# Performance work log

Measured on AMD Instinct MI355X. Metric: run time of the kernel, lower is better.

The kernel has to match this reference:

```python
import jax, jax.numpy as jnp
import numpy as np

EPS = 1e-6
NUM_GROUPS = 32


def setup_inputs() -> dict:
    key = jax.random.key(0)
    ks = jax.random.split(key, 10)
    b, c, h, w = 8, 256, 128, 128
    x = jax.random.normal(ks[0], (b, c, h, w), dtype=jnp.float32)
    gamma = jnp.ones((c,), dtype=jnp.float32)
    beta = jnp.zeros((c,), dtype=jnp.float32)
    Wq = jax.random.normal(ks[1], (c, c), dtype=jnp.float32) * 0.02
    bq = jnp.zeros((c,), dtype=jnp.float32)
    Wk = jax.random.normal(ks[2], (c, c), dtype=jnp.float32) * 0.02
    bk = jnp.zeros((c,), dtype=jnp.float32)
    Wv = jax.random.normal(ks[3], (c, c), dtype=jnp.float32) * 0.02
    bv = jnp.zeros((c,), dtype=jnp.float32)
    Wo = jax.random.normal(ks[4], (c, c), dtype=jnp.float32) * 0.02
    bo = jnp.zeros((c,), dtype=jnp.float32)
    return {"x": x, "gamma": gamma, "beta": beta, "Wq": Wq, "bq": bq,
            "Wk": Wk, "bk": bk, "Wv": Wv, "bv": bv, "Wo": Wo, "bo": bo}


def _group_norm(x, gamma, beta):
    b, c, h, w = x.shape
    g = NUM_GROUPS
    xg = x.reshape(b, g, c // g, h, w)
    mean = jnp.mean(xg, axis=(2, 3, 4), keepdims=True)
    var = jnp.var(xg, axis=(2, 3, 4), keepdims=True)
    xn = ((xg - mean) * jax.lax.rsqrt(var + EPS)).reshape(b, c, h, w)
    return xn * gamma[None, :, None, None] + beta[None, :, None, None]


def reference(x, gamma, beta, Wq, bq, Wk, bk, Wv, bv, Wo, bo):
    b, c, h, w = x.shape
    xn = _group_norm(x, gamma, beta)
    xf = xn.reshape(b, c, h * w)  # [b, c, n]
    # 1x1 convs == channel-mixing matmuls
    Q = jnp.einsum('oc,bcn->bon', Wq, xf) + bq[None, :, None]
    K = jnp.einsum('oc,bcn->bon', Wk, xf) + bk[None, :, None]
    V = jnp.einsum('oc,bcn->bon', Wv, xf) + bv[None, :, None]
    # softmax over the spatial dim n (linear-attention variant)
    Q = jax.nn.softmax(Q, axis=-1)
    K = jax.nn.softmax(K, axis=-1)
    attn = jnp.einsum('bcn,bdn->bcd', Q, K) / jnp.sqrt(jnp.float32(c))  # [b, c, c]
    out = jnp.einsum('bcd,bdn->bcn', attn, V)  # [b, c, n]
    out = jnp.einsum('oc,bcn->bon', Wo, out) + bo[None, :, None]
    return out.reshape(b, c, h, w)
```

## Files before the change

### kernel.cpp

```cpp
#include <hip/hip_runtime.h>
#include <hip/hip_bf16.h>

#define BATCH 8
#define CHN 256
#define HWN 16384
#define EPSV 1e-6f
#define ESCH 32

typedef __attribute__((ext_vector_type(8))) short bf16x8;
typedef __attribute__((ext_vector_type(4))) short s16x4;
typedef __attribute__((ext_vector_type(4))) float f32x4;
typedef __hip_bfloat16 bf16;

__device__ __forceinline__ short f2s(float f){
  union { bf16 h; short s; } u; u.h = __float2bfloat16(f); return u.s;
}
__device__ __forceinline__ float s2f(short s){
  union { unsigned u; float f; } v; v.u = ((unsigned)(unsigned short)s) << 16; return v.f;
}
__device__ __forceinline__ void gload16(const bf16* g, bf16* l){
  __builtin_amdgcn_global_load_lds((const __attribute__((address_space(1))) void*)g,
                                   (__attribute__((address_space(3))) void*)l, 16, 0, 0);
}

__global__ __launch_bounds__(256) void xstats_t(const float* __restrict__ x,
    bf16* __restrict__ xt, float* __restrict__ pst){
  int b = blockIdx.y, n0 = blockIdx.x * 64;
  __shared__ bf16 tile[256][70];
  __shared__ float sg[32], ssg[32];
  int t = threadIdx.x;
  if (t < 32){ sg[t] = 0.f; ssg[t] = 0.f; }
  __syncthreads();
  const float* xb = x + (size_t)b * CHN * HWN;
  #pragma unroll 4
  for (int i = 0; i < 16; i++){
    int c = i * 16 + (t >> 4);
    int nf = (t & 15) * 4;
    float4 v = *(const float4*)(xb + (size_t)c * HWN + n0 + nf);
    tile[c][nf + 0] = __float2bfloat16(v.x);
    tile[c][nf + 1] = __float2bfloat16(v.y);
    tile[c][nf + 2] = __float2bfloat16(v.z);
    tile[c][nf + 3] = __float2bfloat16(v.w);
    float s  = v.x + v.y + v.z + v.w;
    float ss = v.x*v.x + v.y*v.y + v.z*v.z + v.w*v.w;
    s  += __shfl_xor(s, 1);  s  += __shfl_xor(s, 2);
    s  += __shfl_xor(s, 4);  s  += __shfl_xor(s, 8);
    ss += __shfl_xor(ss, 1); ss += __shfl_xor(ss, 2);
    ss += __shfl_xor(ss, 4); ss += __shfl_xor(ss, 8);
    if ((t & 15) == 0){ atomicAdd(&sg[c >> 3], s); atomicAdd(&ssg[c >> 3], ss); }
  }
  __syncthreads();
  bf16* o = xt + (size_t)b * HWN * CHN;
  #pragma unroll 4
  for (int j = 0; j < 64; j++)
    o[(size_t)(n0 + j) * CHN + t] = tile[t][j];
  if (t < 32){
    atomicAdd(&pst[(b * 32 + t) * 2],     sg[t]);
    atomicAdd(&pst[(b * 32 + t) * 2 + 1], ssg[t]);
  }
}

__global__ __launch_bounds__(256) void wprep(const float* __restrict__ Wq,
    const float* __restrict__ Wk, const float* __restrict__ Wv,
    const float* __restrict__ Wo, const float* __restrict__ gamma,
    const float* __restrict__ beta, const float* __restrict__ bv,
    const float* __restrict__ pst, bf16* __restrict__ wqk,
    bf16* __restrict__ wvt, bf16* __restrict__ wob, float* __restrict__ tvb){
  int w = blockIdx.x, b = blockIdx.y, rt = blockIdx.z, t = threadIdx.x;
  if (w == 3 && b != 0) return;
  const float* W = (w == 0) ? Wq : ((w == 1) ? Wk : ((w == 2) ? Wv : Wo));
  __shared__ float a_s[256], sh_s[256];
  __shared__ float racc[16];
  {
    int bg = b * 32 + (t >> 3);
    float m   = pst[bg * 2] * (1.f / 131072.f);
    float var = pst[bg * 2 + 1] * (1.f / 131072.f) - m * m;
    float r = rsqrtf(var + EPSV);
    float a = r * gamma[t];
    a_s[t] = a;
    sh_s[t] = beta[t] - m * a;
  }
  if (t < 16) racc[t] = 0.f;
  __syncthreads();
  float mya = a_s[t], mysh = sh_s[t];
  int lane = t & 63;
  bf16* wo_qk = wqk + ((size_t)b << 17) + ((size_t)w << 16);
  bf16* wo_v  = wvt + ((size_t)b << 16);
  #pragma unroll
  for (int jj = 0; jj < 16; jj++){
    int j = rt * 16 + jj;
    float wv_ = W[j * 256 + t];
    if (w < 2) wo_qk[j * 256 + t] = __float2bfloat16(wv_ * mya);
    else if (w == 3) wob[j * 256 + t] = __float2bfloat16(wv_);
    else {
      wo_v[(size_t)t * 256 + j] = __float2bfloat16(wv_ * mya);
      float p = wv_ * mysh;
      p += __shfl_xor(p, 1);  p += __shfl_xor(p, 2);  p += __shfl_xor(p, 4);
      p += __shfl_xor(p, 8);  p += __shfl_xor(p, 16); p += __shfl_xor(p, 32);
      if (lane == 0) atomicAdd(&racc[jj], p);
    }
  }
  if (w == 2){
    __syncthreads();
    if (t < 16) tvb[b * 256 + rt * 16 + t] = racc[t] + bv[rt * 16 + t];
  }
}

__global__ __launch_bounds__(256, 2) void qk_gemm(const bf16* __restrict__ wqk,
    const bf16* __restrict__ xt, bf16* __restrict__ Eout,
    float* __restrict__ sums){
  __shared__ bf16 lW[2][256 * 32];
  __shared__ bf16 lX[2][128 * 32];
  int t = threadIdx.x, nt = blockIdx.x, h = blockIdx.y, b = blockIdx.z;
  const bf16* Wb = wqk + ((size_t)b << 17) + ((size_t)h << 16);
  const bf16* Xb = xt + (size_t)b * HWN * CHN + (size_t)(nt * 128) * CHN;
  int lane = t & 63, w = t >> 6, r = lane & 15, kc = lane >> 4;
  f32x4 acc[8][4] = {};

  auto stage = [&](int buf, int k0){
    #pragma unroll
    for (int rep = 0; rep < 4; rep++){
      int c = t + rep * 256; int row = c >> 2;
      int off = ((c & 3) ^ ((c >> 3) & 3)) * 8;
      gload16(Wb + (size_t)row * 256 + k0 + off, &lW[buf][c * 8]);
    }
    #pragma unroll
    for (int rep = 0; rep < 2; rep++){
      int c = t + rep * 256; int row = c >> 2;
      int off = ((c & 3) ^ ((c >> 3) & 3)) * 8;
      gload16(Xb + (size_t)row * 256 + k0 + off, &lX[buf][c * 8]);
    }
  };

  stage(0, 0);
  __syncthreads();
  int cur = 0;
  int slot8 = (kc ^ ((r >> 1) & 3)) * 8;
  for (int ks = 0; ks < 8; ks++){
    if (ks < 7) stage(cur ^ 1, (ks + 1) * 32);
    bf16x8 af[8], bfv[4];
    #pragma unroll
    for (int i = 0; i < 8; i++)
      af[i] = *(const bf16x8*)&lX[cur][(i * 16 + r) * 32 + slot8];
    #pragma unroll
    for (int f = 0; f < 4; f++)
      bfv[f] = *(const bf16x8*)&lW[cur][(w * 64 + f * 16 + r) * 32 + slot8];
    #pragma unroll
    for (int i = 0; i < 8; i++)
      #pragma unroll
      for (int f = 0; f < 4; f++)
        acc[i][f] = __builtin_amdgcn_mfma_f32_16x16x32_bf16(af[i], bfv[f], acc[i][f], 0, 0, 0);
    __syncthreads();
    cur ^= 1;
  }

  char* scrB = (char*)&lW[0][0];
  float colp[4] = {0.f, 0.f, 0.f, 0.f};
  int base_row = (h ? 2048 : 0) + b * 256;
  #pragma unroll
  for (int p = 0; p < 2; p++){
    __syncthreads();
    #pragma unroll
    for (int fl = 0; fl < 2; fl++){
      int f = p * 2 + fl;
      int ri = w * 32 + fl * 16 + r;
      int key = (ri & 7) << 4;
      #pragma unroll
      for (int i = 0; i < 8; i++){
        s16x4 pk;
        #pragma unroll
        for (int j = 0; j < 4; j++){
          float e = __expf(acc[i][f][j]);
          colp[f] += e;
          pk[j] = f2s(e);
        }
        *(s16x4*)(scrB + ri * 256 + ((i * 32 + kc * 8) ^ key)) = pk;
      }
    }
    __syncthreads();
    #pragma unroll
    for (int ps = 0; ps < 8; ps++){
      int c = t + ps * 256;
      int ri = c >> 4, q = c & 15;
      int key = (ri & 7) << 4;
      int4 v = *(const int4*)(scrB + ri * 256 + ((q * 16) ^ key));
      int wrow = (ri >> 5) * 64 + (p * 2 + ((ri >> 4) & 1)) * 16 + (ri & 15);
      *(int4*)&Eout[(size_t)(base_row + wrow) * HWN + nt * 128 + q * 8] = v;
    }
  }
  #pragma unroll
  for (int f = 0; f < 4; f++){
    float v = colp[f];
    v += __shfl_xor(v, 16); v += __shfl_xor(v, 32);
    if (lane < 16)
      atomicAdd(&sums[base_row + w * 64 + f * 16 + r], v);
  }
}

__global__ __launch_bounds__(256, 2) void es_gemm(const bf16* __restrict__ Ek,
    const bf16* __restrict__ Eq, float* __restrict__ spart){
  __shared__ bf16 lA[2][128 * 32];
  __shared__ bf16 lB[2][256 * 32];
  int t = threadIdx.x, ch = blockIdx.x, mt = blockIdx.y, z = blockIdx.z;
  const bf16* At = Ek + (size_t)z * 256 * HWN + (size_t)(mt * 128) * HWN + ch * 512;
  const bf16* Bt = Eq + (size_t)z * 256 * HWN + ch * 512;
  f32x4 acc[4][8] = {};
  int lane = t & 63, w = t >> 6, r = lane & 15, kc = lane >> 4;
  int ng = w >> 1, cg = w & 1;

  auto stage = [&](int buf, int k0){
    #pragma unroll
    for (int rep = 0; rep < 2; rep++){
      int c = t + rep * 256; int row = c >> 2;
      int off = ((c & 3) ^ ((c >> 3) & 3)) * 8;
      gload16(At + (size_t)row * HWN + k0 + off, &lA[buf][c * 8]);
    }
    #pragma unroll
    for (int rep = 0; rep < 4; rep++){
      int c = t + rep * 256; int row = c >> 2;
      int off = ((c & 3) ^ ((c >> 3) & 3)) * 8;
      gload16(Bt + (size_t)row * HWN + k0 + off, &lB[buf][c * 8]);
    }
  };

  stage(0, 0);
  __syncthreads();
  int cur = 0;
  int slot8 = (kc ^ ((r >> 1) & 3)) * 8;
  for (int ks = 0; ks < 16; ks++){
    if (ks < 15) stage(cur ^ 1, (ks + 1) * 32);
    bf16x8 af[4], bfv[8];
    #pragma unroll
    for (int i = 0; i < 4; i++)
      af[i] = *(const bf16x8*)&lA[cur][(ng * 64 + i * 16 + r) * 32 + slot8];
    #pragma unroll
    for (int f = 0; f < 8; f++)
      bfv[f] = *(const bf16x8*)&lB[cur][(cg * 128 + f * 16 + r) * 32 + slot8];
    #pragma unroll
    for (int i = 0; i < 4; i++)
      #pragma unroll
      for (int f = 0; f < 8; f++)
        acc[i][f] = __builtin_amdgcn_mfma_f32_16x16x32_bf16(af[i], bfv[f], acc[i][f], 0, 0, 0);
    __syncthreads();
    cur ^= 1;
  }

  float* sp = spart + ((size_t)(z * ESCH + ch) << 16);
  #pragma unroll
  for (int f = 0; f < 8; f++){
    int q = cg * 128 + f * 16 + r;
    #pragma unroll
    for (int i = 0; i < 4; i++){
      int k0i = mt * 128 + ng * 64 + i * 16 + kc * 4;
      *(f32x4*)&sp[q * 256 + k0i] = acc[i][f];
    }
  }
}

__global__ void reduce_S(const float* __restrict__ sp, float* __restrict__ S){
  size_t i = ((size_t)blockIdx.x * 256 + threadIdx.x) * 4;
  size_t b = i >> 16, cd = i & 65535;
  float4 s = {0.f, 0.f, 0.f, 0.f};
  #pragma unroll
  for (int ch = 0; ch < ESCH; ch++){
    float4 v = *(const float4*)&sp[((b * ESCH + ch) << 16) + cd];
    s.x += v.x; s.y += v.y; s.z += v.z; s.w += v.w;
  }
  *(float4*)&S[i] = s;
}

__global__ __launch_bounds__(256) void scaleS_t(const float* __restrict__ S,
    const float* __restrict__ sums, bf16* __restrict__ T1t){
  int id = blockIdx.x, b = blockIdx.y;
  int dt = id >> 2, ct = id & 3, t = threadIdx.x;
  __shared__ float tile[64][65];
  __shared__ float sq_s[64], sk_s[64];
  if (t < 64)       sq_s[t]      = 0.0625f / sums[b * 256 + ct * 64 + t];
  else if (t < 128) sk_s[t - 64] = 1.f / sums[2048 + b * 256 + dt * 64 + (t - 64)];
  const float* Sb = S + ((size_t)b << 16);
  #pragma unroll
  for (int i = 0; i < 4; i++){
    int c_l = i * 16 + (t >> 4);
    int d_l0 = (t & 15) * 4;
    float4 v = *(const float4*)&Sb[(size_t)(ct * 64 + c_l) * 256 + dt * 64 + d_l0];
    tile[d_l0 + 0][c_l] = v.x;
    tile[d_l0 + 1][c_l] = v.y;
    tile[d_l0 + 2][c_l] = v.z;
    tile[d_l0 + 3][c_l] = v.w;
  }
  __syncthreads();
  bf16* Tb = T1t + ((size_t)b << 16);
  #pragma unroll
  for (int i = 0; i < 4; i++){
    int d_l = i * 16 + (t >> 4);
    int c_l0 = (t & 15) * 4;
    s16x4 pk;
    #pragma unroll
    for (int jj = 0; jj < 4; jj++)
      pk[jj] = f2s(tile[d_l][c_l0 + jj] * sq_s[c_l0 + jj] * sk_s[d_l]);
    *(s16x4*)&Tb[(size_t)(dt * 64 + d_l) * 256 + ct * 64 + c_l0] = pk;
  }
}

__global__ __launch_bounds__(256, 2) void nt_gemm(const bf16* __restrict__ A,
    const bf16* __restrict__ B, bf16* __restrict__ out,
    long Asb, long Bsb, long Osb){
  __shared__ bf16 lA[2][256 * 32];
  __shared__ bf16 lB[2][128 * 32];
  int t = threadIdx.x, mt = blockIdx.x, b = blockIdx.y;
  const bf16* Ab = A + (size_t)b * Asb;
  const bf16* Bb = B + (size_t)b * Bsb + (size_t)(mt * 128) * 256;
  bf16* Ob = out + (size_t)b * Osb + (size_t)(mt * 128) * 256;
  int lane = t & 63, w = t >> 6, r = lane & 15, kc = lane >> 4;
  f32x4 acc[16][2] = {};

  auto stage = [&](int buf, int k0){
    #pragma unroll
    for (int rep = 0; rep < 4; rep++){
      int c = t + rep * 256; int row = c >> 2, off = (c & 3) * 8;
      gload16(Ab + (size_t)row * 256 + k0 + off, &lA[buf][c * 8]);
    }
    #pragma unroll
    for (int rep = 0; rep < 2; rep++){
      int c = t + rep * 256; int row = c >> 2, off = (c & 3) * 8;
      gload16(Bb + (size_t)row * 256 + k0 + off, &lB[buf][c * 8]);
    }
  };

  stage(0, 0);
  __syncthreads();
  int cur = 0;
  for (int ks = 0; ks < 8; ks++){
    if (ks < 7) stage(cur ^ 1, (ks + 1) * 32);
    bf16x8 bfv[2];
    #pragma unroll
    for (int f = 0; f < 2; f++)
      bfv[f] = *(const bf16x8*)&lB[cur][(w * 32 + f * 16 + r) * 32 + kc * 8];
    #pragma unroll
    for (int i = 0; i < 16; i++){
      bf16x8 af = *(const bf16x8*)&lA[cur][(i * 16 + r) * 32 + kc * 8];
      acc[i][0] = __builtin_amdgcn_mfma_f32_16x16x32_bf16(af, bfv[0], acc[i][0], 0, 0, 0);
      acc[i][1] = __builtin_amdgcn_mfma_f32_16x16x32_bf16(af, bfv[1], acc[i][1], 0, 0, 0);
    }
    __syncthreads();
    cur ^= 1;
  }

  #pragma unroll
  for (int f = 0; f < 2; f++){
    int bcol = w * 32 + f * 16 + r;
    #pragma unroll
    for (int i = 0; i < 16; i++){
      s16x4 pk;
      #pragma unroll
      for (int j = 0; j < 4; j++) pk[j] = f2s(acc[i][f][j]);
      *(s16x4*)&Ob[(size_t)bcol * 256 + i * 16 + kc * 4] = pk;
    }
  }
}

__global__ __launch_bounds__(256) void beff_k(const bf16* __restrict__ Mbf,
    const float* __restrict__ tvb, const float* __restrict__ bo,
    float* __restrict__ beff){
  int b = blockIdx.x, t = threadIdx.x;
  __shared__ float tv[256];
  tv[t] = tvb[b * 256 + t];
  __syncthreads();
  const bf16* Mr = Mbf + ((size_t)b << 16) + (size_t)t * 256;
  float s = 0.f;
  #pragma unroll
  for (int k = 0; k < 32; k++){
    bf16x8 v = *(const bf16x8*)&Mr[k * 8];
    #pragma unroll
    for (int e = 0; e < 8; e++) s += s2f(v[e]) * tv[k * 8 + e];
  }
  beff[b * 256 + t] = s + bo[t];
}

__global__ __launch_bounds__(256, 2) void out_gemm(const bf16* __restrict__ xt,
    const bf16* __restrict__ Nb, const float* __restrict__ beff,
    float* __restrict__ out){
  __shared__ bf16 lA[2][128 * 32];
  __shared__ bf16 lB[2][256 * 32];
  int t = threadIdx.x, nt = blockIdx.x, z = blockIdx.y;
  const bf16* At = xt + (size_t)z * HWN * CHN + (size_t)(nt * 128) * CHN;
  const bf16* Bt = Nb + (size_t)z * 65536;
  f32x4 acc[4][8] = {};
  int lane = t & 63, w = t >> 6, r = lane & 15, kc = lane >> 4;
  int ng = w >> 1, cg = w & 1;

  auto stage = [&](int buf, int k0){
    #pragma unroll
    for (int rep = 0; rep < 2; rep++){
      int c = t + rep * 256; int row = c >> 2;
      int off = ((c & 3) ^ ((c >> 3) & 3)) * 8;
      gload16(At + (size_t)row * 256 + k0 + off, &lA[buf][c * 8]);
    }
    #pragma unroll
    for (int rep = 0; rep < 4; rep++){
      int c = t + rep * 256; int row = c >> 2;
      int off = ((c & 3) ^ ((c >> 3) & 3)) * 8;
      gload16(Bt + (size_t)row * 256 + k0 + off, &lB[buf][c * 8]);
    }
  };

  stage(0, 0);
  __syncthreads();
  int cur = 0;
  int slot8 = (kc ^ ((r >> 1) & 3)) * 8;
  for (int ks = 0; ks < 8; ks++){
    if (ks < 7) stage(cur ^ 1, (ks + 1) * 32);
    bf16x8 af[4], bfv[8];
    #pragma unroll
    for (int i = 0; i < 4; i++)
      af[i] = *(const bf16x8*)&lA[cur][(ng * 64 + i * 16 + r) * 32 + slot8];
    #pragma unroll
    for (int f = 0; f < 8; f++)
      bfv[f] = *(const bf16x8*)&lB[cur][(cg * 128 + f * 16 + r) * 32 + slot8];
    #pragma unroll
    for (int i = 0; i < 4; i++)
      #pragma unroll
      for (int f = 0; f < 8; f++)
        acc[i][f] = __builtin_amdgcn_mfma_f32_16x16x32_bf16(af[i], bfv[f], acc[i][f], 0, 0, 0);
    __syncthreads();
    cur ^= 1;
  }

  float* ob = out + (size_t)z * CHN * HWN;
  #pragma unroll
  for (int f = 0; f < 8; f++){
    int o = cg * 128 + f * 16 + r;
    float bb = beff[z * 256 + o];
    #pragma unroll
    for (int i = 0; i < 4; i++){
      int n0 = nt * 128 + ng * 64 + i * 16 + kc * 4;
      float4 st = { acc[i][f][0] + bb, acc[i][f][1] + bb,
                    acc[i][f][2] + bb, acc[i][f][3] + bb };
      *(float4*)&ob[(size_t)o * HWN + n0] = st;
    }
  }
}

extern "C" void kernel_launch(void* const* d_in, const int* in_sizes, int n_in,
                              void* d_out, int out_size, void* d_ws, size_t ws_size,
                              hipStream_t stream){
  const float* x     = (const float*)d_in[0];
  const float* gamma = (const float*)d_in[1];
  const float* beta  = (const float*)d_in[2];
  const float* Wq    = (const float*)d_in[3];
  const float* Wk    = (const float*)d_in[5];
  const float* Wv    = (const float*)d_in[7];
  const float* bv    = (const float*)d_in[8];
  const float* Wo    = (const float*)d_in[9];
  const float* bo    = (const float*)d_in[10];

  char* ws = (char*)d_ws;
  bf16*  xt    = (bf16*) (ws + 0);
  float* spart = (float*)(ws + 67108864);
  bf16*  wqk   = (bf16*) (ws + 134217728);
  bf16*  wob   = (bf16*) (ws + 136314880);
  bf16*  wvt   = (bf16*) (ws + 136445952);
  float* S     = (float*)(ws + 137494528);
  bf16*  T1t   = (bf16*) (ws + 139591680);
  bf16*  Mbf   = (bf16*) (ws + 140640256);
  bf16*  Nb    = (bf16*) (ws + 141688832);
  float* sums  = (float*)(ws + 142737408);
  float* pst   = (float*)(ws + 142753792);
  float* tvb   = (float*)(ws + 142755840);
  float* beff  = (float*)(ws + 142764032);

  bf16* Qb = (bf16*)d_out;
  bf16* Kb = Qb + (size_t)2048 * HWN;

  hipMemsetAsync(sums, 0, 4096 * sizeof(float), stream);
  hipMemsetAsync(pst,  0,  512 * sizeof(float), stream);

  xstats_t<<<dim3(256, 8), dim3(256), 0, stream>>>(x, xt, pst);
  wprep<<<dim3(4, 8, 16), dim3(256), 0, stream>>>(Wq, Wk, Wv, Wo, gamma, beta,
                                                  bv, pst, wqk, wvt, wob, tvb);
  qk_gemm<<<dim3(128, 2, 8), dim3(256), 0, stream>>>(wqk, xt, Qb, sums);
  es_gemm<<<dim3(ESCH, 2, 8), dim3(256), 0, stream>>>(Kb, Qb, spart);
  reduce_S<<<dim3(512), dim3(256), 0, stream>>>(spart, S);
  scaleS_t<<<dim3(16, 8), dim3(256), 0, stream>>>(S, sums, T1t);
  nt_gemm<<<dim3(2, 8), dim3(256), 0, stream>>>(T1t, wob, Mbf, 65536L, 0L, 65536L);
  beff_k<<<dim3(8), dim3(256), 0, stream>>>(Mbf, tvb, bo, beff);
  nt_gemm<<<dim3(2, 8), dim3(256), 0, stream>>>(wvt, Mbf, Nb, 65536L, 65536L, 65536L);
  out_gemm<<<dim3(128, 8), dim3(256), 0, stream>>>(xt, Nb, beff, (float*)d_out);
}
```

Measured before the change: 293.1 us.

## Vectorize transpose stores in xstats and triple-buffer qk_gemm loads

The stats/transpose kernel now handles 32 spatial positions per block. It writes bf16 into an XOR-swizzled shared scratch and emits 16-byte coalesced stores of the transposed tile, where before it did per-element 2-byte stores. It also replaces the shared-memory atomics with full-wavefront shuffle reductions. The QK GEMM moves from double to triple buffering, prefetching two K-steps ahead and using explicit vmcnt waits with raw barriers instead of __syncthreads. The cost is more LDS per block, which may limit occupancy under launch_bounds(256,2), and fragile manual wait counts.

```diff
diff --git a/kernel.cpp b/kernel.cpp
--- a/kernel.cpp
+++ b/kernel.cpp
@@ -25,38 +25,42 @@
 
 __global__ __launch_bounds__(256) void xstats_t(const float* __restrict__ x,
     bf16* __restrict__ xt, float* __restrict__ pst){
-  int b = blockIdx.y, n0 = blockIdx.x * 64;
-  __shared__ bf16 tile[256][70];
+  int b = blockIdx.y, n0 = blockIdx.x * 32;
+  __shared__ char scr[32 * 512];
   __shared__ float sg[32], ssg[32];
-  int t = threadIdx.x;
-  if (t < 32){ sg[t] = 0.f; ssg[t] = 0.f; }
-  __syncthreads();
+  int t = threadIdx.x, lane = t & 63, w = t >> 6;
   const float* xb = x + (size_t)b * CHN * HWN;
-  #pragma unroll 4
-  for (int i = 0; i < 16; i++){
-    int c = i * 16 + (t >> 4);
-    int nf = (t & 15) * 4;
+  #pragma unroll
+  for (int i = 0; i < 8; i++){
+    int c = i * 32 + (t >> 3);
+    int nf = (t & 7) * 4;
     float4 v = *(const float4*)(xb + (size_t)c * HWN + n0 + nf);
-    tile[c][nf + 0] = __float2bfloat16(v.x);
-    tile[c][nf + 1] = __float2bfloat16(v.y);
-    tile[c][nf + 2] = __float2bfloat16(v.z);
-    tile[c][nf + 3] = __float2bfloat16(v.w);
+    #pragma unroll
+    for (int j = 0; j < 4; j++){
+      int row = nf + j;
+      float e = j == 0 ? v.x : (j == 1 ? v.y : (j == 2 ? v.z : v.w));
+      *(short*)(scr + row * 512 + ((c * 2) ^ ((row & 7) << 4))) = f2s(e);
+    }
     float s  = v.x + v.y + v.z + v.w;
     float ss = v.x*v.x + v.y*v.y + v.z*v.z + v.w*v.w;
-    s  += __shfl_xor(s, 1);  s  += __shfl_xor(s, 2);
-    s  += __shfl_xor(s, 4);  s  += __shfl_xor(s, 8);
-    ss += __shfl_xor(ss, 1); ss += __shfl_xor(ss, 2);
-    ss += __shfl_xor(ss, 4); ss += __shfl_xor(ss, 8);
-    if ((t & 15) == 0){ atomicAdd(&sg[c >> 3], s); atomicAdd(&ssg[c >> 3], ss); }
-  }
-  __syncthreads();
-  bf16* o = xt + (size_t)b * HWN * CHN;
-  #pragma unroll 4
-  for (int j = 0; j < 64; j++)
-    o[(size_t)(n0 + j) * CHN + t] = tile[t][j];
+    s  += __shfl_xor(s, 1);  s  += __shfl_xor(s, 2);  s  += __shfl_xor(s, 4);
+    s  += __shfl_xor(s, 8);  s  += __shfl_xor(s, 16); s  += __shfl_xor(s, 32);
+    ss += __shfl_xor(ss, 1); ss += __shfl_xor(ss, 2); ss += __shfl_xor(ss, 4);
+    ss += __shfl_xor(ss, 8); ss += __shfl_xor(ss, 16); ss += __shfl_xor(ss, 32);
+    if (lane == 0){ sg[i * 4 + w] = s; ssg[i * 4 + w] = ss; }
+  }
+  __syncthreads();
   if (t < 32){
     atomicAdd(&pst[(b * 32 + t) * 2],     sg[t]);
     atomicAdd(&pst[(b * 32 + t) * 2 + 1], ssg[t]);
+  }
+  bf16* o = xt + (size_t)b * HWN * CHN + (size_t)n0 * CHN;
+  #pragma unroll
+  for (int p = 0; p < 4; p++){
+    int idx = p * 256 + t;
+    int n = idx >> 5, cq = idx & 31;
+    int4 v = *(const int4*)(scr + n * 512 + ((cq * 16) ^ ((n & 7) << 4)));
+    *(int4*)&o[n * 256 + cq * 8] = v;
   }
 }
 
@@ -109,8 +113,8 @@
 __global__ __launch_bounds__(256, 2) void qk_gemm(const bf16* __restrict__ wqk,
     const bf16* __restrict__ xt, bf16* __restrict__ Eout,
     float* __restrict__ sums){
-  __shared__ bf16 lW[2][256 * 32];
-  __shared__ bf16 lX[2][128 * 32];
+  __shared__ bf16 lW[3][256 * 32];
+  __shared__ bf16 lX[3][128 * 32];
   int t = threadIdx.x, nt = blockIdx.x, h = blockIdx.y, b = blockIdx.z;
   const bf16* Wb = wqk + ((size_t)b << 17) + ((size_t)h << 16);
   const bf16* Xb = xt + (size_t)b * HWN * CHN + (size_t)(nt * 128) * CHN;
@@ -133,11 +137,14 @@
   };
 
   stage(0, 0);
-  __syncthreads();
-  int cur = 0;
+  stage(1, 32);
+  asm volatile("s_waitcnt vmcnt(6)" ::: "memory");
+  __builtin_amdgcn_s_barrier();
   int slot8 = (kc ^ ((r >> 1) & 3)) * 8;
+  #pragma unroll
   for (int ks = 0; ks < 8; ks++){
-    if (ks < 7) stage(cur ^ 1, (ks + 1) * 32);
+    int cur = ks % 3;
+    if (ks < 6) stage((ks + 2) % 3, (ks + 2) * 32);
     bf16x8 af[8], bfv[4];
     #pragma unroll
     for (int i = 0; i < 8; i++)
@@ -150,8 +157,11 @@
       #pragma unroll
       for (int f = 0; f < 4; f++)
         acc[i][f] = __builtin_amdgcn_mfma_f32_16x16x32_bf16(af[i], bfv[f], acc[i][f], 0, 0, 0);
-    __syncthreads();
-    cur ^= 1;
+    if (ks < 7){
+      if (ks < 6) asm volatile("s_waitcnt vmcnt(6)" ::: "memory");
+      else        asm volatile("s_waitcnt vmcnt(0)" ::: "memory");
+      __builtin_amdgcn_s_barrier();
+    }
   }
 
   char* scrB = (char*)&lW[0][0];
@@ -475,7 +485,7 @@
   hipMemsetAsync(sums, 0, 4096 * sizeof(float), stream);
   hipMemsetAsync(pst,  0,  512 * sizeof(float), stream);
 
-  xstats_t<<<dim3(256, 8), dim3(256), 0, stream>>>(x, xt, pst);
+  xstats_t<<<dim3(512, 8), dim3(256), 0, stream>>>(x, xt, pst);
   wprep<<<dim3(4, 8, 16), dim3(256), 0, stream>>>(Wq, Wk, Wv, Wo, gamma, beta,
                                                   bv, pst, wqk, wvt, wob, tvb);
   qk_gemm<<<dim3(128, 2, 8), dim3(256), 0, stream>>>(wqk, xt, Qb, sums);
```

After: 311.7 us. +6.3%, slower.
